# Kernel tuning notes

Hardware: AMD Instinct MI355X
Metric: run time of the kernel (lower is better)

## Reference

```python
import jax, jax.numpy as jnp
import numpy as np

N = 400000      # simplices (edges of the complexes)
E = 2400000     # nnz of each Laplacian
F_IN = 32
H = 64
KAPPA = 3
G = 512         # graphs in batch
N_OUT = 8
EPS = 1e-5


def spmm(edge_index, edge_values, x, n):
    # y[i] = sum_e val_e * x[j],  i = edge_index[0], j = edge_index[1]
    msg = edge_values[:, None] * x[edge_index[1]]
    return jax.ops.segment_sum(msg, edge_index[0], num_segments=n)


def sc_layer(x, li, lv, ui, uv, Wl, bl, Wu, bu, Wh, bh):
    # SCNN layer: z_low + z_up + z_har (aggr_x fused in)
    n = x.shape[0]
    z = x @ Wh + bh                       # harmonic / identity term
    xl = x
    for k in range(KAPPA):
        xl = spmm(li, lv, xl, n)          # L_low^{k+1} x
        z = z + xl @ Wl[k] + bl[k]
    xu = x
    for k in range(KAPPA):
        xu = spmm(ui, uv, xu, n)          # L_up^{k+1} x
        z = z + xu @ Wu[k] + bu[k]
    return z


def batch_norm(x, gamma, beta):
    mean = jnp.mean(x, axis=0)
    var = jnp.mean((x - mean) ** 2, axis=0)   # biased, as torch BN training
    return (x - mean) * jax.lax.rsqrt(var + EPS) * gamma + beta


def setup_inputs() -> dict:
    key = jax.random.key(0)
    ks = jax.random.split(key, 32)
    s_in = 1.0 / np.sqrt(F_IN)
    s_h = 1.0 / np.sqrt(H)
    inp = {
        "x": jax.random.normal(ks[0], (N, F_IN), jnp.float32),
        "lower_edge_index": jax.random.randint(ks[1], (2, E), 0, N),
        "lower_edge_values": jax.random.normal(ks[2], (E,), jnp.float32),
        "upper_edge_index": jax.random.randint(ks[3], (2, E), 0, N),
        "upper_edge_values": jax.random.normal(ks[4], (E,), jnp.float32),
        "batch_index": jnp.sort(jax.random.randint(ks[5], (N,), 0, G)),
        # layer 0 (F_IN -> H)
        "l0_Wl": jax.random.normal(ks[6], (KAPPA, F_IN, H), jnp.float32) * s_in,
        "l0_bl": jnp.zeros((KAPPA, H), jnp.float32),
        "l0_Wu": jax.random.normal(ks[7], (KAPPA, F_IN, H), jnp.float32) * s_in,
        "l0_bu": jnp.zeros((KAPPA, H), jnp.float32),
        "l0_Wh": jax.random.normal(ks[8], (F_IN, H), jnp.float32) * s_in,
        "l0_bh": jnp.zeros((H,), jnp.float32),
        # layer 1 (H -> H)
        "l1_Wl": jax.random.normal(ks[9], (KAPPA, H, H), jnp.float32) * s_h,
        "l1_bl": jnp.zeros((KAPPA, H), jnp.float32),
        "l1_Wu": jax.random.normal(ks[10], (KAPPA, H, H), jnp.float32) * s_h,
        "l1_bu": jnp.zeros((KAPPA, H), jnp.float32),
        "l1_Wh": jax.random.normal(ks[11], (H, H), jnp.float32) * s_h,
        "l1_bh": jnp.zeros((H,), jnp.float32),
        # batch norms
        "bn0_g": jnp.ones((H,), jnp.float32),
        "bn0_b": jnp.zeros((H,), jnp.float32),
        "bn1_g": jnp.ones((H,), jnp.float32),
        "bn1_b": jnp.zeros((H,), jnp.float32),
        # output MLP [2H, H, N_OUT]
        "mlp_W1": jax.random.normal(ks[12], (2 * H, H), jnp.float32) / np.sqrt(2 * H),
        "mlp_b1": jnp.zeros((H,), jnp.float32),
        "mlp_W2": jax.random.normal(ks[13], (H, N_OUT), jnp.float32) * s_h,
        "mlp_b2": jnp.zeros((N_OUT,), jnp.float32),
    }
    return inp


def reference(x, lower_edge_values, upper_edge_values,
              l0_Wl, l0_bl, l0_Wu, l0_bu, l0_Wh, l0_bh,
              l1_Wl, l1_bl, l1_Wu, l1_bu, l1_Wh, l1_bh,
              bn0_g, bn0_b, bn1_g, bn1_b,
              mlp_W1, mlp_b1, mlp_W2, mlp_b2,
              lower_edge_index, upper_edge_index, batch_index):
    li, ui, bi = lower_edge_index, upper_edge_index, batch_index
    lv, uv = lower_edge_values, upper_edge_values

    h = sc_layer(x, li, lv, ui, uv, l0_Wl, l0_bl, l0_Wu, l0_bu, l0_Wh, l0_bh)
    h = jax.nn.elu(batch_norm(h, bn0_g, bn0_b))
    h = sc_layer(h, li, lv, ui, uv, l1_Wl, l1_bl, l1_Wu, l1_bu, l1_Wh, l1_bh)
    h = jax.nn.elu(batch_norm(h, bn1_g, bn1_b))

    # global max pool + global mean pool per graph
    gmax = jax.ops.segment_max(h, bi, num_segments=G)
    gsum = jax.ops.segment_sum(h, bi, num_segments=G)
    cnt = jax.ops.segment_sum(jnp.ones((h.shape[0],), h.dtype), bi, num_segments=G)
    gmean = gsum / jnp.maximum(cnt, 1.0)[:, None]
    g = jax.nn.elu(jnp.concatenate([gmax, gmean], axis=1))  # [G, 2H]

    # MLP [2H -> H -> N_OUT]
    g = jax.nn.relu(g @ mlp_W1 + mlp_b1)
    return g @ mlp_W2 + mlp_b2
```

## Files before the change

kernel.cpp:

```cpp
#include <hip/hip_runtime.h>
#include <hip/hip_bf16.h>
#include <math.h>

#define N_SIMP 400000
#define E_NNZ  2400000
#define FIN    32
#define HDIM   64
#define KAPPA  3
#define G_NUM  512
#define NOUT   8
#define BN_EPS 1e-5

#define NDIG_HALF 391
#define NDIG      782
#define P1_EDGES  16384
#define P1_BLOCKS 293
#define P1_T      1024
#define P1_EPT    16
#define P2_CAP    7168
#define P2_T      512
#define P2_ITERS  14

typedef __hip_bfloat16 bf16;
typedef _Float16 f16;
typedef short s8v __attribute__((ext_vector_type(8)));
typedef ushort u8v __attribute__((ext_vector_type(8)));
typedef _Float16 h8v __attribute__((ext_vector_type(8)));
typedef float f4v __attribute__((ext_vector_type(4)));

__device__ __forceinline__ float elu_f(float x) {
    return x > 0.f ? x : expm1f(x);
}
__device__ __forceinline__ float bf2f(ushort u) {
    return __uint_as_float(((unsigned int)u) << 16);
}
__device__ __forceinline__ ushort f2bf(float f) {
    bf16 h = (bf16)f;
    return *(ushort*)&h;
}


__global__ __launch_bounds__(P1_T, 1) void p1_sort_kernel(
        const int* __restrict__ eiL, const float* __restrict__ lv,
        const int* __restrict__ eiU, const float* __restrict__ uv,
        int* __restrict__ ccnt, int* __restrict__ bofsv,
        int2* __restrict__ coarse) {
    __shared__ int2 rec[P1_EDGES];
    __shared__ int h[NDIG];
    __shared__ int hscan[P1_T];
    int t = threadIdx.x;
    for (int j = t; j < NDIG; j += P1_T) h[j] = 0;
    __syncthreads();
    int base_i = blockIdx.x * P1_EDGES;
    int key[P1_EPT], val[P1_EPT], dg[P1_EPT];
#pragma unroll
    for (int k = 0; k < P1_EPT; ++k) {
        int i = base_i + k * P1_T + t;
        int dd = -1;
        if (i < 2 * E_NNZ) {
            int row, col;
            float v;
            if (i < E_NNZ) {
                row = eiL[i]; col = eiL[E_NNZ + i]; v = lv[i];
                dd = row >> 10;
            } else {
                int e = i - E_NNZ;
                row = eiU[e]; col = eiU[E_NNZ + e]; v = uv[e];
                dd = NDIG_HALF + (row >> 10);
            }
            key[k] = ((row & 1023) << 22) | col;
            val[k] = __float_as_int(v);
            atomicAdd(&h[dd], 1);
        }
        dg[k] = dd;
    }
    __syncthreads();
    int cv = (t < NDIG) ? h[t] : 0;
    hscan[t] = cv;
    __syncthreads();
    for (int off = 1; off < P1_T; off <<= 1) {
        int x = (t >= off) ? hscan[t - off] : 0;
        __syncthreads();
        hscan[t] += x;
        __syncthreads();
    }
    if (t < NDIG) {
        int ex = hscan[t] - cv;
        ccnt[blockIdx.x * NDIG + t] = cv;
        bofsv[blockIdx.x * NDIG + t] = ex;
        h[t] = ex;
    }
    __syncthreads();
#pragma unroll
    for (int k = 0; k < P1_EPT; ++k) {
        if (dg[k] >= 0) {
            int pos = atomicAdd(&h[dg[k]], 1);
            rec[pos] = make_int2(key[k], val[k]);
        }
    }
    __syncthreads();
    int2* dst = coarse + (size_t)blockIdx.x * P1_EDGES;
    int nrec = 2 * E_NNZ - base_i;
    if (nrec > P1_EDGES) nrec = P1_EDGES;
    for (int j = t; j < nrec; j += P1_T) dst[j] = rec[j];
}

__global__ void digit_total_kernel(const int* __restrict__ cnt, int* __restrict__ tot) {
    int d = blockIdx.x * 256 + threadIdx.x;
    if (d >= NDIG) return;
    int run = 0;
    for (int b = 0; b < P1_BLOCKS; ++b) run += cnt[b * NDIG + d];
    tot[d] = run;
}

__global__ __launch_bounds__(1024) void scan_base_kernel(int* __restrict__ tot) {
    __shared__ int s[1024];
    int t = threadIdx.x;
    int v = (t < NDIG) ? tot[t] : 0;
    s[t] = v;
    __syncthreads();
    for (int off = 1; off < 1024; off <<= 1) {
        int x = (t >= off) ? s[t - off] : 0;
        __syncthreads();
        s[t] += x;
        __syncthreads();
    }
    if (t < NDIG) tot[t] = s[t] - v;
    if (t == 1023) tot[NDIG] = s[1023];
}


__global__ __launch_bounds__(P2_T) void p2_build_kernel(
        const int2* __restrict__ coarse, const int* __restrict__ ccnt,
        const int* __restrict__ bofsv, const int* __restrict__ basev,
        int* __restrict__ rpL, int* __restrict__ rpU,
        int2* __restrict__ edgeL, int2* __restrict__ edgeU) {
    __shared__ int pk[P2_CAP];
    __shared__ int vl[P2_CAP];
    __shared__ int hist[1024];
    __shared__ int sc[P2_T];
    __shared__ int fo[P1_BLOCKS];
    __shared__ int stot;
    int d = blockIdx.x;
    int t = threadIdx.x;
    int len = 0, ofs = 0;
    if (t < P1_BLOCKS) { len = ccnt[t * NDIG + d]; ofs = bofsv[t * NDIG + d]; }
    sc[t] = len;
    __syncthreads();
    for (int off = 1; off < P2_T; off <<= 1) {
        int x = (t >= off) ? sc[t - off] : 0;
        __syncthreads();
        sc[t] += x;
        __syncthreads();
    }
    if (t < P1_BLOCKS) { fo[t] = sc[t] - len; hist[t] = len; hist[512 + t] = ofs; }
    if (t == P1_BLOCKS - 1) stot = sc[t];
    __syncthreads();
    int sz = stot;
    if (sz > P2_CAP) sz = P2_CAP;
    int wv = t >> 6, lane = t & 63;
    for (int b = wv; b < P1_BLOCKS; b += P2_T / 64) {
        int L = hist[b], O = hist[512 + b], F = fo[b];
        const int2* sp = coarse + (size_t)b * P1_EDGES + O;
        for (int j = lane; j < L; j += 64) {
            int dst2 = F + j;
            if (dst2 < P2_CAP) {
                int2 r = sp[j];
                pk[dst2] = r.x;
                vl[dst2] = r.y;
            }
        }
    }
    __syncthreads();
    hist[t] = 0;
    hist[t + P2_T] = 0;
    __syncthreads();
    int myrank[P2_ITERS];
#pragma unroll
    for (int k = 0; k < P2_ITERS; ++k) {
        int j = k * P2_T + t;
        myrank[k] = (j < sz) ? atomicAdd(&hist[((unsigned)pk[j]) >> 22], 1) : 0;
    }
    __syncthreads();
    int h0 = hist[2 * t], h1 = hist[2 * t + 1];
    sc[t] = h0 + h1;
    __syncthreads();
    for (int off = 1; off < P2_T; off <<= 1) {
        int x = (t >= off) ? sc[t - off] : 0;
        __syncthreads();
        sc[t] += x;
        __syncthreads();
    }
    int pbase = sc[t] - (h0 + h1);
    __syncthreads();
    hist[2 * t] = pbase;
    hist[2 * t + 1] = pbase + h0;
    int which = (d >= NDIG_HALF);
    int lbase = basev[d] - (which ? E_NNZ : 0);
    int rowbase = (which ? d - NDIG_HALF : d) << 10;
    int* rp = which ? rpU : rpL;
    int r0 = rowbase + 2 * t, r1 = r0 + 1;
    if (r0 < N_SIMP) rp[r0] = lbase + pbase;
    if (r1 < N_SIMP) rp[r1] = lbase + pbase + h0;
    __syncthreads();
    int2* eout = which ? edgeU : edgeL;
#pragma unroll
    for (int k = 0; k < P2_ITERS; ++k) {
        int j = k * P2_T + t;
        if (j < sz) {
            unsigned p = (unsigned)pk[j];
            int pos = lbase + hist[p >> 22] + myrank[k];
            eout[pos] = make_int2((int)(p & 0x3FFFFF), vl[j]);
        }
    }
}


__global__ void combine_bias_kernel(const float* __restrict__ bh,
                                    const float* __restrict__ bl,
                                    const float* __restrict__ bu,
                                    float* __restrict__ out) {
    int h = threadIdx.x;
    float acc = bh[h];
    for (int k = 0; k < KAPPA; ++k) acc += bl[k * HDIM + h] + bu[k * HDIM + h];
    out[h] = acc;
}

__global__ void f32_to_bf16_kernel(const float* __restrict__ in, bf16* __restrict__ out) {
    int idx = blockIdx.x * 256 + threadIdx.x;
    float4 v = ((const float4*)in)[idx];
    ushort4 w;
    w.x = f2bf(v.x); w.y = f2bf(v.y); w.z = f2bf(v.z); w.w = f2bf(v.w);
    ((ushort4*)out)[idx] = w;
}

__global__ void wtrans_all_kernel(const float* __restrict__ s0, const float* __restrict__ s1,
                                  const float* __restrict__ s2, const float* __restrict__ s3,
                                  const float* __restrict__ s4, const float* __restrict__ s5,
                                  ushort* __restrict__ wt) {
    int idx = blockIdx.x * 256 + threadIdx.x;
    const float* src; int off;
    if (idx < 2048)       { src = s0; off = 0; }
    else if (idx < 6144)  { src = s1; off = 2048; }
    else if (idx < 12288) { src = s2; off = 6144; }
    else if (idx < 18432) { src = s3; off = 12288; }
    else if (idx < 30720) { src = s4; off = 18432; }
    else                  { src = s5; off = 30720; }
    int rel = idx - off;
    int frag = rel >> 9;
    int r = rel & 511;
    int lane = r >> 3, j = r & 7;
    int q = lane >> 4, n = lane & 15;
    int ch = frag >> 2, nblk = frag & 3;
    int k = ch * 32 + q * 8 + j;
    int nout = nblk * 16 + n;
    wt[idx] = f2bf(src[k * 64 + nout]);
}


__global__ void spmm32_kernel(const int* __restrict__ rp, const int2* __restrict__ edge,
                              const bf16* __restrict__ srcb, int src_stride,
                              bf16* __restrict__ dstb) {
    const ushort* src = (const ushort*)srcb;
    ushort* dst = (ushort*)dstb;
    int tid = threadIdx.x;
    int lane = tid & 63;
    int wv = tid >> 6;
    int grp = lane >> 2;
    int li = lane & 3;
    int row = blockIdx.x * 64 + wv * 16 + grp;
    int s = rp[row];
    int e = (row == N_SIMP - 1) ? E_NNZ : rp[row + 1];
    int deg = e - s;
    float a[8] = {0.f, 0.f, 0.f, 0.f, 0.f, 0.f, 0.f, 0.f};
    if (deg > 0) {
        int2 ed[8];
#pragma unroll
        for (int t = 0; t < 8; ++t) {
            int j = s + t;
            ed[t] = edge[(j < e) ? j : (e - 1)];
        }
        u8v xs[8];
#pragma unroll
        for (int t = 0; t < 8; ++t)
            xs[t] = *(const u8v*)(src + (size_t)ed[t].x * src_stride + li * 8);
#pragma unroll
        for (int t = 0; t < 8; ++t) {
            float v = (t < deg) ? __int_as_float(ed[t].y) : 0.f;
#pragma unroll
            for (int c = 0; c < 8; ++c) a[c] += v * bf2f(xs[t][c]);
        }
        for (int j = s + 8; j < e; j += 4) {
            int2 e2[4];
#pragma unroll
            for (int t = 0; t < 4; ++t) {
                int jj = j + t;
                e2[t] = edge[(jj < e) ? jj : (e - 1)];
            }
            u8v x2[4];
#pragma unroll
            for (int t = 0; t < 4; ++t)
                x2[t] = *(const u8v*)(src + (size_t)e2[t].x * src_stride + li * 8);
#pragma unroll
            for (int t = 0; t < 4; ++t) {
                float v = (j + t < e) ? __int_as_float(e2[t].y) : 0.f;
#pragma unroll
                for (int c = 0; c < 8; ++c) a[c] += v * bf2f(x2[t][c]);
            }
        }
    }
    u8v w;
#pragma unroll
    for (int c = 0; c < 8; ++c) w[c] = f2bf(a[c]);
    *(u8v*)(dst + (size_t)row * 32 + li * 8) = w;
}

__global__ void spmm64_kernel(const int* __restrict__ rp, const int2* __restrict__ edge,
                              const bf16* __restrict__ srcb, bf16* __restrict__ dstb) {
    const ushort* src = (const ushort*)srcb;
    ushort* dst = (ushort*)dstb;
    int tid = threadIdx.x;
    int lane = tid & 63;
    int wv = tid >> 6;
    int grp = lane >> 3;
    int li = lane & 7;
    int row = blockIdx.x * 32 + wv * 8 + grp;
    int s = rp[row];
    int e = (row == N_SIMP - 1) ? E_NNZ : rp[row + 1];
    int deg = e - s;
    float a[8] = {0.f, 0.f, 0.f, 0.f, 0.f, 0.f, 0.f, 0.f};
    if (deg > 0) {
        int2 ed[8];
#pragma unroll
        for (int t = 0; t < 8; ++t) {
            int j = s + t;
            ed[t] = edge[(j < e) ? j : (e - 1)];
        }
        u8v xs[8];
#pragma unroll
        for (int t = 0; t < 8; ++t)
            xs[t] = *(const u8v*)(src + (size_t)ed[t].x * 64 + li * 8);
#pragma unroll
        for (int t = 0; t < 8; ++t) {
            float v = (t < deg) ? __int_as_float(ed[t].y) : 0.f;
#pragma unroll
            for (int c = 0; c < 8; ++c) a[c] += v * bf2f(xs[t][c]);
        }
        for (int j = s + 8; j < e; j += 4) {
            int2 e2[4];
#pragma unroll
            for (int t = 0; t < 4; ++t) {
                int jj = j + t;
                e2[t] = edge[(jj < e) ? jj : (e - 1)];
            }
            u8v x2[4];
#pragma unroll
            for (int t = 0; t < 4; ++t)
                x2[t] = *(const u8v*)(src + (size_t)e2[t].x * 64 + li * 8);
#pragma unroll
            for (int t = 0; t < 4; ++t) {
                float v = (j + t < e) ? __int_as_float(e2[t].y) : 0.f;
#pragma unroll
                for (int c = 0; c < 8; ++c) a[c] += v * bf2f(x2[t][c]);
            }
        }
    }
    u8v w;
#pragma unroll
    for (int c = 0; c < 8; ++c) w[c] = f2bf(a[c]);
    *(u8v*)(dst + (size_t)row * 64 + li * 8) = w;
}


template <int NCH, int NCH1, bool INIT>
__global__ __launch_bounds__(256) void mfma_gemm_kernel(
        const ushort* __restrict__ s0, int st0,
        const ushort* __restrict__ s1, int st1,
        const ushort* __restrict__ s2, int st2,
        const ushort* __restrict__ s3, int st3,
        const ushort* __restrict__ s4, int st4,
        const ushort* __restrict__ s5, int st5,
        const ushort* __restrict__ Wt1,
        const ushort* __restrict__ Wt2,
        const float* __restrict__ bias,
        f16* __restrict__ z) {
    int tid = threadIdx.x;
    int wv = tid >> 6, lane = tid & 63;
    int quad = lane >> 4, n = lane & 15;
    int rowbase = blockIdx.x * 64 + wv * 16;
    int arow = rowbase + n;

    f4v acc0 = {0.f, 0.f, 0.f, 0.f};
    f4v acc1 = {0.f, 0.f, 0.f, 0.f};
    f4v acc2 = {0.f, 0.f, 0.f, 0.f};
    f4v acc3 = {0.f, 0.f, 0.f, 0.f};

#pragma unroll
    for (int ch = 0; ch < NCH; ++ch) {
        const ushort* sp = (ch == 0) ? s0 : (ch == 1) ? s1 : (ch == 2) ? s2
                         : (ch == 3) ? s3 : (ch == 4) ? s4 : s5;
        int st = (ch == 0) ? st0 : (ch == 1) ? st1 : (ch == 2) ? st2
               : (ch == 3) ? st3 : (ch == 4) ? st4 : st5;
        const ushort* wb = (ch < NCH1) ? (Wt1 + (size_t)ch * 2048)
                                       : (Wt2 + (size_t)(ch - NCH1) * 2048);
        s8v a = *(const s8v*)(sp + (size_t)arow * st + quad * 8);
        const ushort* wq = wb + lane * 8;
        s8v b0 = *(const s8v*)(wq + 0 * 512);
        s8v b1 = *(const s8v*)(wq + 1 * 512);
        s8v b2 = *(const s8v*)(wq + 2 * 512);
        s8v b3 = *(const s8v*)(wq + 3 * 512);
        acc0 = __builtin_amdgcn_mfma_f32_16x16x32_bf16(a, b0, acc0, 0, 0, 0);
        acc1 = __builtin_amdgcn_mfma_f32_16x16x32_bf16(a, b1, acc1, 0, 0, 0);
        acc2 = __builtin_amdgcn_mfma_f32_16x16x32_bf16(a, b2, acc2, 0, 0, 0);
        acc3 = __builtin_amdgcn_mfma_f32_16x16x32_bf16(a, b3, acc3, 0, 0, 0);
    }
#pragma unroll
    for (int r = 0; r < 4; ++r) {
        int orow = rowbase + quad * 4 + r;
        f16* zp = z + (size_t)orow * 64 + n;
        if (INIT) {
            zp[0]  = (f16)(bias[n]      + acc0[r]);
            zp[16] = (f16)(bias[16 + n] + acc1[r]);
            zp[32] = (f16)(bias[32 + n] + acc2[r]);
            zp[48] = (f16)(bias[48 + n] + acc3[r]);
        } else {
            zp[0]  = (f16)((float)zp[0]  + acc0[r]);
            zp[16] = (f16)((float)zp[16] + acc1[r]);
            zp[32] = (f16)((float)zp[32] + acc2[r]);
            zp[48] = (f16)((float)zp[48] + acc3[r]);
        }
    }
}


__global__ void bn_stats_kernel(const f16* __restrict__ z, double* __restrict__ stats) {
    __shared__ float ss[256 * 8], qq[256 * 8];
    int tid = threadIdx.x;
    const h8v* z8 = (const h8v*)z;
    const int total8 = N_SIMP * HDIM / 8;
    float fs[8] = {0, 0, 0, 0, 0, 0, 0, 0};
    float fq[8] = {0, 0, 0, 0, 0, 0, 0, 0};
    for (int i = blockIdx.x * 256 + tid; i < total8; i += (int)gridDim.x * 256) {
        h8v v = z8[i];
#pragma unroll
        for (int c = 0; c < 8; ++c) {
            float f = (float)v[c];
            fs[c] += f;
            fq[c] += f * f;
        }
    }
#pragma unroll
    for (int c = 0; c < 8; ++c) { ss[tid * 8 + c] = fs[c]; qq[tid * 8 + c] = fq[c]; }
    __syncthreads();
    if (tid < 64) {
        int sel = tid >> 3, slot = tid & 7;
        double a = 0.0, b = 0.0;
#pragma unroll 8
        for (int k = 0; k < 32; ++k) {
            int t = sel + (k << 3);
            a += (double)ss[t * 8 + slot];
            b += (double)qq[t * 8 + slot];
        }
        atomicAdd(&stats[tid], a);
        atomicAdd(&stats[64 + tid], b);
    }
}

__global__ void bn_elu_bf16_kernel(const f16* __restrict__ z, const double* __restrict__ stats,
                                   const float* __restrict__ gamma, const float* __restrict__ beta,
                                   bf16* __restrict__ out) {
    __shared__ float scale_s[64], shift_s[64];
    int tid = threadIdx.x;
    if (tid < 64) {
        double mean = stats[tid] / (double)N_SIMP;
        double var = stats[64 + tid] / (double)N_SIMP - mean * mean;
        double sc = (double)gamma[tid] / sqrt(var + BN_EPS);
        scale_s[tid] = (float)sc;
        shift_s[tid] = (float)((double)beta[tid] - mean * sc);
    }
    __syncthreads();
    const h8v* z8 = (const h8v*)z;
    u8v* o8 = (u8v*)out;
    const int total8 = N_SIMP * HDIM / 8;
    int hb = (tid & 7) * 8;
    for (int i = blockIdx.x * 256 + tid; i < total8; i += (int)gridDim.x * 256) {
        h8v v = z8[i];
        u8v w;
#pragma unroll
        for (int c = 0; c < 8; ++c)
            w[c] = f2bf(elu_f((float)v[c] * scale_s[hb + c] + shift_s[hb + c]));
        o8[i] = w;
    }
}

__global__ void pool_bn_kernel(const f16* __restrict__ zbuf, const int* __restrict__ bidx,
                               const double* __restrict__ stats,
                               const float* __restrict__ gamma, const float* __restrict__ beta,
                               float* __restrict__ gbuf) {
    __shared__ float scale_s[64], shift_s[64];
    __shared__ float pmax[256 * 8], psum[256 * 8];
    int tid = threadIdx.x;
    if (tid < 64) {
        double mean = stats[tid] / (double)N_SIMP;
        double var = stats[64 + tid] / (double)N_SIMP - mean * mean;
        double sc = (double)gamma[tid] / sqrt(var + BN_EPS);
        scale_s[tid] = (float)sc;
        shift_s[tid] = (float)((double)beta[tid] - mean * sc);
    }
    __syncthreads();
    int g = blockIdx.x;
    int lo = 0, hi = N_SIMP;
    while (lo < hi) { int mid = (lo + hi) >> 1; if (bidx[mid] < g) lo = mid + 1; else hi = mid; }
    int start = lo;
    hi = N_SIMP;
    while (lo < hi) { int mid = (lo + hi) >> 1; if (bidx[mid] < g + 1) lo = mid + 1; else hi = mid; }
    int end = lo;
    int li = tid & 7;
    int rr = tid >> 3;
    const h8v* z8 = (const h8v*)zbuf;
    float mx[8], sm[8];
#pragma unroll
    for (int c = 0; c < 8; ++c) { mx[c] = -INFINITY; sm[c] = 0.f; }
    float sc8[8], sh8[8];
#pragma unroll
    for (int c = 0; c < 8; ++c) { sc8[c] = scale_s[li * 8 + c]; sh8[c] = shift_s[li * 8 + c]; }
    for (int i = start + rr; i < end; i += 32) {
        h8v v = z8[(size_t)i * 8 + li];
#pragma unroll
        for (int c = 0; c < 8; ++c) {
            float y = elu_f((float)v[c] * sc8[c] + sh8[c]);
            mx[c] = fmaxf(mx[c], y);
            sm[c] += y;
        }
    }
#pragma unroll
    for (int c = 0; c < 8; ++c) { pmax[tid * 8 + c] = mx[c]; psum[tid * 8 + c] = sm[c]; }
    __syncthreads();
    if (tid < 64) {
        int sel = tid >> 3, slot = tid & 7;
        float m = -INFINITY, s = 0.f;
#pragma unroll 8
        for (int k = 0; k < 32; ++k) {
            int t = k * 8 + sel;
            m = fmaxf(m, pmax[t * 8 + slot]);
            s += psum[t * 8 + slot];
        }
        int cnt = end - start;
        float mean = s / fmaxf((float)cnt, 1.f);
        gbuf[g * 128 + tid] = elu_f(m);
        gbuf[g * 128 + 64 + tid] = elu_f(mean);
    }
}

__global__ void mlp_kernel(const float* __restrict__ gbuf, const float* __restrict__ W1,
                           const float* __restrict__ b1, const float* __restrict__ W2,
                           const float* __restrict__ b2, float* __restrict__ out) {
    __shared__ float gs[128];
    __shared__ float hs[64];
    int g = blockIdx.x, tid = threadIdx.x;
    gs[tid] = gbuf[g * 128 + tid];
    gs[64 + tid] = gbuf[g * 128 + 64 + tid];
    __syncthreads();
    float acc = b1[tid];
#pragma unroll
    for (int k = 0; k < 128; ++k) acc += gs[k] * W1[k * 64 + tid];
    hs[tid] = fmaxf(acc, 0.f);
    __syncthreads();
    if (tid < 8) {
        float o = b2[tid];
#pragma unroll
        for (int k = 0; k < 64; ++k) o += hs[k] * W2[k * 8 + tid];
        out[g * 8 + tid] = o;
    }
}


extern "C" void kernel_launch(void* const* d_in, const int* in_sizes, int n_in,
                              void* d_out, int out_size, void* d_ws, size_t ws_size,
                              hipStream_t stream) {
    const float* x     = (const float*)d_in[0];
    const int*   li    = (const int*)d_in[1];
    const float* lv    = (const float*)d_in[2];
    const int*   ui    = (const int*)d_in[3];
    const float* uv    = (const float*)d_in[4];
    const int*   bidx  = (const int*)d_in[5];
    const float* l0_Wl = (const float*)d_in[6];
    const float* l0_bl = (const float*)d_in[7];
    const float* l0_Wu = (const float*)d_in[8];
    const float* l0_bu = (const float*)d_in[9];
    const float* l0_Wh = (const float*)d_in[10];
    const float* l0_bh = (const float*)d_in[11];
    const float* l1_Wl = (const float*)d_in[12];
    const float* l1_bl = (const float*)d_in[13];
    const float* l1_Wu = (const float*)d_in[14];
    const float* l1_bu = (const float*)d_in[15];
    const float* l1_Wh = (const float*)d_in[16];
    const float* l1_bh = (const float*)d_in[17];
    const float* bn0_g = (const float*)d_in[18];
    const float* bn0_b = (const float*)d_in[19];
    const float* bn1_g = (const float*)d_in[20];
    const float* bn1_b = (const float*)d_in[21];
    const float* mW1   = (const float*)d_in[22];
    const float* mb1   = (const float*)d_in[23];
    const float* mW2   = (const float*)d_in[24];
    const float* mb2   = (const float*)d_in[25];
    float* out = (float*)d_out;

    char* base = (char*)d_ws;
    f16*   z     = (f16*)base;
    bf16*  h0bf  = (bf16*)(base + 51200000ull);
    bf16*  g1    = (bf16*)(base + 102400000ull);
    bf16*  g2    = (bf16*)(base + 153600000ull);
    int2*  edgeL = (int2*)(base + 204800000ull);
    int2*  edgeU = (int2*)(base + 224000000ull);
    int*   rpL   = (int*)(base + 243200000ull);
    int*   rpU   = (int*)(base + 244800032ull);
    double* stats = (double*)(base + 246404160ull);
    float* cbias  = (float*)(base + 246405184ull);
    float* gbuf   = (float*)(base + 246405440ull);
    ushort* wt    = (ushort*)(base + 246667584ull);

    int2* coarse = (int2*)base;
    int*  basev  = (int*)(base + 38500000ull);
    int*  ccnt   = (int*)(base + 51200000ull);
    int*  bofsv  = (int*)(base + 52200000ull);

    bf16* xbf  = g1;
    bf16* cAL  = g1 + (size_t)N_SIMP * 32;
    bf16* cBL  = g2;
    bf16* cCL  = g2 + (size_t)N_SIMP * 32;
    bf16* cAU  = h0bf;
    bf16* cBU  = h0bf + (size_t)N_SIMP * 32;
    bf16* cCU  = g1;

    ushort* wt_l0h = wt;
    ushort* wt_l1h = wt + 2048;
    ushort* wt_l0l = wt + 6144;
    ushort* wt_l0u = wt + 12288;
    ushort* wt_l1l = wt + 18432;
    ushort* wt_l1u = wt + 30720;

    const int SP32_BLOCKS = N_SIMP / 64;
    const int SP64_BLOCKS = N_SIMP / 32;
    const int MF_BLOCKS   = N_SIMP / 64;

    wtrans_all_kernel<<<168, 256, 0, stream>>>(l0_Wh, l1_Wh, l0_Wl, l0_Wu, l1_Wl, l1_Wu, wt);
    f32_to_bf16_kernel<<<N_SIMP * 32 / 4 / 256, 256, 0, stream>>>(x, xbf);

    p1_sort_kernel<<<P1_BLOCKS, P1_T, 0, stream>>>(li, lv, ui, uv, ccnt, bofsv, coarse);
    digit_total_kernel<<<(NDIG + 255) / 256, 256, 0, stream>>>(ccnt, basev);
    scan_base_kernel<<<1, 1024, 0, stream>>>(basev);
    p2_build_kernel<<<NDIG, P2_T, 0, stream>>>(coarse, ccnt, bofsv, basev,
                                               rpL, rpU, edgeL, edgeU);

    const ushort* xbfu = (const ushort*)xbf;
    const ushort* h0u  = (const ushort*)h0bf;
    const ushort* g1u  = (const ushort*)g1;
    const ushort* g2u  = (const ushort*)g2;

    combine_bias_kernel<<<1, 64, 0, stream>>>(l0_bh, l0_bl, l0_bu, cbias);
    mfma_gemm_kernel<1, 1, true><<<MF_BLOCKS, 256, 0, stream>>>(
        xbfu, 32, nullptr, 0, nullptr, 0, nullptr, 0, nullptr, 0, nullptr, 0,
        wt_l0h, wt_l0h, cbias, z);

    spmm32_kernel<<<SP32_BLOCKS, 256, 0, stream>>>(rpL, edgeL, xbf, 32, cAL);
    spmm32_kernel<<<SP32_BLOCKS, 256, 0, stream>>>(rpL, edgeL, cAL, 32, cBL);
    spmm32_kernel<<<SP32_BLOCKS, 256, 0, stream>>>(rpL, edgeL, cBL, 32, cCL);
    spmm32_kernel<<<SP32_BLOCKS, 256, 0, stream>>>(rpU, edgeU, xbf, 32, cAU);
    spmm32_kernel<<<SP32_BLOCKS, 256, 0, stream>>>(rpU, edgeU, cAU, 32, cBU);
    spmm32_kernel<<<SP32_BLOCKS, 256, 0, stream>>>(rpU, edgeU, cBU, 32, cCU);
    mfma_gemm_kernel<6, 3, false><<<MF_BLOCKS, 256, 0, stream>>>(
        (const ushort*)cAL, 32, (const ushort*)cBL, 32, (const ushort*)cCL, 32,
        (const ushort*)cAU, 32, (const ushort*)cBU, 32, (const ushort*)cCU, 32,
        wt_l0l, wt_l0u, nullptr, z);

    (void)hipMemsetAsync(stats, 0, 128 * sizeof(double), stream);
    bn_stats_kernel<<<1024, 256, 0, stream>>>(z, stats);
    bn_elu_bf16_kernel<<<1024, 256, 0, stream>>>(z, stats, bn0_g, bn0_b, h0bf);

    combine_bias_kernel<<<1, 64, 0, stream>>>(l1_bh, l1_bl, l1_bu, cbias);

    spmm64_kernel<<<SP64_BLOCKS, 256, 0, stream>>>(rpL, edgeL, h0bf, g1);
    spmm64_kernel<<<SP64_BLOCKS, 256, 0, stream>>>(rpL, edgeL, g1, g2);
    mfma_gemm_kernel<6, 2, true><<<MF_BLOCKS, 256, 0, stream>>>(
        h0u, 64, h0u + 32, 64, g1u, 64, g1u + 32, 64, g2u, 64, g2u + 32, 64,
        wt_l1h, wt_l1l, cbias, z);
    spmm64_kernel<<<SP64_BLOCKS, 256, 0, stream>>>(rpL, edgeL, g2, g1);
    spmm64_kernel<<<SP64_BLOCKS, 256, 0, stream>>>(rpU, edgeU, h0bf, g2);
    mfma_gemm_kernel<4, 2, false><<<MF_BLOCKS, 256, 0, stream>>>(
        g1u, 64, g1u + 32, 64, g2u, 64, g2u + 32, 64, nullptr, 0, nullptr, 0,
        wt_l1l + 4 * 2048, wt_l1u, nullptr, z);
    spmm64_kernel<<<SP64_BLOCKS, 256, 0, stream>>>(rpU, edgeU, g2, g1);
    spmm64_kernel<<<SP64_BLOCKS, 256, 0, stream>>>(rpU, edgeU, g1, g2);
    mfma_gemm_kernel<4, 4, false><<<MF_BLOCKS, 256, 0, stream>>>(
        g1u, 64, g1u + 32, 64, g2u, 64, g2u + 32, 64, nullptr, 0, nullptr, 0,
        wt_l1u + 2 * 2048, wt_l1u + 2 * 2048, nullptr, z);

    (void)hipMemsetAsync(stats, 0, 128 * sizeof(double), stream);
    bn_stats_kernel<<<1024, 256, 0, stream>>>(z, stats);

    pool_bn_kernel<<<G_NUM, 256, 0, stream>>>(z, bidx, stats, bn1_g, bn1_b, gbuf);
    mlp_kernel<<<G_NUM, 64, 0, stream>>>(gbuf, mW1, mb1, mW2, mb2, out);
}
```

Measured before the change: 1.197 ms.

## Fuse BN statistics into final GEMM epilogues and halve sort block size

Batch-norm sum and sum-of-squares are now accumulated in the epilogue of the last MFMA GEMM of each layer, using shared-memory float atomics and then global double atomics. This drops both bn_stats_kernel launches and their full re-read of z. Separately, the coarse sort pass uses 8192-edge blocks (586 blocks) without the single-block occupancy bound, and the build kernel gathers each bucket with 8-lane groups. The fused stats add atomic contention in every GEMM block, and the smaller sort blocks double the per-digit bucket metadata.

New measurement: 1.368 ms. +14.3%, slower.

```diff
diff --git a/kernel.cpp b/kernel.cpp
--- a/kernel.cpp
+++ b/kernel.cpp
@@ -13,10 +13,10 @@
 
 #define NDIG_HALF 391
 #define NDIG      782
-#define P1_EDGES  16384
-#define P1_BLOCKS 293
+#define P1_EDGES  8192
+#define P1_BLOCKS 586
 #define P1_T      1024
-#define P1_EPT    16
+#define P1_EPT    8
 #define P2_CAP    7168
 #define P2_T      512
 #define P2_ITERS  14
@@ -40,7 +40,7 @@
 }
 
 
-__global__ __launch_bounds__(P1_T, 1) void p1_sort_kernel(
+__global__ __launch_bounds__(P1_T) void p1_sort_kernel(
         const int* __restrict__ eiL, const float* __restrict__ lv,
         const int* __restrict__ eiU, const float* __restrict__ uv,
         int* __restrict__ ccnt, int* __restrict__ bofsv,
@@ -139,13 +139,17 @@
     __shared__ int vl[P2_CAP];
     __shared__ int hist[1024];
     __shared__ int sc[P2_T];
+    __shared__ int flen[P1_BLOCKS];
+    __shared__ int fofs[P1_BLOCKS];
     __shared__ int fo[P1_BLOCKS];
     __shared__ int stot;
     int d = blockIdx.x;
     int t = threadIdx.x;
-    int len = 0, ofs = 0;
-    if (t < P1_BLOCKS) { len = ccnt[t * NDIG + d]; ofs = bofsv[t * NDIG + d]; }
-    sc[t] = len;
+    int f0 = 2 * t, f1 = 2 * t + 1;
+    int L0 = 0, L1 = 0, O0 = 0, O1 = 0;
+    if (f0 < P1_BLOCKS) { L0 = ccnt[f0 * NDIG + d]; O0 = bofsv[f0 * NDIG + d]; }
+    if (f1 < P1_BLOCKS) { L1 = ccnt[f1 * NDIG + d]; O1 = bofsv[f1 * NDIG + d]; }
+    sc[t] = L0 + L1;
     __syncthreads();
     for (int off = 1; off < P2_T; off <<= 1) {
         int x = (t >= off) ? sc[t - off] : 0;
@@ -153,16 +157,19 @@
         sc[t] += x;
         __syncthreads();
     }
-    if (t < P1_BLOCKS) { fo[t] = sc[t] - len; hist[t] = len; hist[512 + t] = ofs; }
-    if (t == P1_BLOCKS - 1) stot = sc[t];
+    int pb = sc[t] - (L0 + L1);
+    if (f0 < P1_BLOCKS) { flen[f0] = L0; fofs[f0] = O0; fo[f0] = pb; }
+    if (f1 < P1_BLOCKS) { flen[f1] = L1; fofs[f1] = O1; fo[f1] = pb + L0; }
+    if (t == P2_T - 1) stot = sc[t];
     __syncthreads();
     int sz = stot;
     if (sz > P2_CAP) sz = P2_CAP;
     int wv = t >> 6, lane = t & 63;
-    for (int b = wv; b < P1_BLOCKS; b += P2_T / 64) {
-        int L = hist[b], O = hist[512 + b], F = fo[b];
+    int grp8 = lane >> 3, l8 = lane & 7;
+    for (int b = wv * 8 + grp8; b < P1_BLOCKS; b += 64) {
+        int L = flen[b], O = fofs[b], F = fo[b];
         const int2* sp = coarse + (size_t)b * P1_EDGES + O;
-        for (int j = lane; j < L; j += 64) {
+        for (int j = l8; j < L; j += 8) {
             int dst2 = F + j;
             if (dst2 < P2_CAP) {
                 int2 r = sp[j];
@@ -372,7 +379,7 @@
 }
 
 
-template <int NCH, int NCH1, bool INIT>
+template <int NCH, int NCH1, bool INIT, bool STATS>
 __global__ __launch_bounds__(256) void mfma_gemm_kernel(
         const ushort* __restrict__ s0, int st0,
         const ushort* __restrict__ s1, int st1,
@@ -383,12 +390,19 @@
         const ushort* __restrict__ Wt1,
         const ushort* __restrict__ Wt2,
         const float* __restrict__ bias,
+        double* __restrict__ stats,
         f16* __restrict__ z) {
+    __shared__ float s_sum[64], s_sq[64];
     int tid = threadIdx.x;
     int wv = tid >> 6, lane = tid & 63;
     int quad = lane >> 4, n = lane & 15;
     int rowbase = blockIdx.x * 64 + wv * 16;
     int arow = rowbase + n;
+
+    if (STATS) {
+        if (tid < 64) { s_sum[tid] = 0.f; s_sq[tid] = 0.f; }
+        __syncthreads();
+    }
 
     f4v acc0 = {0.f, 0.f, 0.f, 0.f};
     f4v acc1 = {0.f, 0.f, 0.f, 0.f};
@@ -414,57 +428,47 @@
         acc2 = __builtin_amdgcn_mfma_f32_16x16x32_bf16(a, b2, acc2, 0, 0, 0);
         acc3 = __builtin_amdgcn_mfma_f32_16x16x32_bf16(a, b3, acc3, 0, 0, 0);
     }
+    float fs[4] = {0.f, 0.f, 0.f, 0.f};
+    float fq[4] = {0.f, 0.f, 0.f, 0.f};
 #pragma unroll
     for (int r = 0; r < 4; ++r) {
         int orow = rowbase + quad * 4 + r;
         f16* zp = z + (size_t)orow * 64 + n;
+        f16 w0, w1, w2, w3;
         if (INIT) {
-            zp[0]  = (f16)(bias[n]      + acc0[r]);
-            zp[16] = (f16)(bias[16 + n] + acc1[r]);
-            zp[32] = (f16)(bias[32 + n] + acc2[r]);
-            zp[48] = (f16)(bias[48 + n] + acc3[r]);
+            w0 = (f16)(bias[n]      + acc0[r]);
+            w1 = (f16)(bias[16 + n] + acc1[r]);
+            w2 = (f16)(bias[32 + n] + acc2[r]);
+            w3 = (f16)(bias[48 + n] + acc3[r]);
         } else {
-            zp[0]  = (f16)((float)zp[0]  + acc0[r]);
-            zp[16] = (f16)((float)zp[16] + acc1[r]);
-            zp[32] = (f16)((float)zp[32] + acc2[r]);
-            zp[48] = (f16)((float)zp[48] + acc3[r]);
-        }
-    }
-}
-
-
-__global__ void bn_stats_kernel(const f16* __restrict__ z, double* __restrict__ stats) {
-    __shared__ float ss[256 * 8], qq[256 * 8];
-    int tid = threadIdx.x;
-    const h8v* z8 = (const h8v*)z;
-    const int total8 = N_SIMP * HDIM / 8;
-    float fs[8] = {0, 0, 0, 0, 0, 0, 0, 0};
-    float fq[8] = {0, 0, 0, 0, 0, 0, 0, 0};
-    for (int i = blockIdx.x * 256 + tid; i < total8; i += (int)gridDim.x * 256) {
-        h8v v = z8[i];
-#pragma unroll
-        for (int c = 0; c < 8; ++c) {
-            float f = (float)v[c];
-            fs[c] += f;
-            fq[c] += f * f;
-        }
-    }
-#pragma unroll
-    for (int c = 0; c < 8; ++c) { ss[tid * 8 + c] = fs[c]; qq[tid * 8 + c] = fq[c]; }
-    __syncthreads();
-    if (tid < 64) {
-        int sel = tid >> 3, slot = tid & 7;
-        double a = 0.0, b = 0.0;
-#pragma unroll 8
-        for (int k = 0; k < 32; ++k) {
-            int t = sel + (k << 3);
-            a += (double)ss[t * 8 + slot];
-            b += (double)qq[t * 8 + slot];
-        }
-        atomicAdd(&stats[tid], a);
-        atomicAdd(&stats[64 + tid], b);
-    }
-}
+            w0 = (f16)((float)zp[0]  + acc0[r]);
+            w1 = (f16)((float)zp[16] + acc1[r]);
+            w2 = (f16)((float)zp[32] + acc2[r]);
+            w3 = (f16)((float)zp[48] + acc3[r]);
+        }
+        zp[0] = w0; zp[16] = w1; zp[32] = w2; zp[48] = w3;
+        if (STATS) {
+            float v0 = (float)w0, v1 = (float)w1, v2 = (float)w2, v3 = (float)w3;
+            fs[0] += v0; fq[0] += v0 * v0;
+            fs[1] += v1; fq[1] += v1 * v1;
+            fs[2] += v2; fq[2] += v2 * v2;
+            fs[3] += v3; fq[3] += v3 * v3;
+        }
+    }
+    if (STATS) {
+#pragma unroll
+        for (int k = 0; k < 4; ++k) {
+            atomicAdd(&s_sum[k * 16 + n], fs[k]);
+            atomicAdd(&s_sq[k * 16 + n], fq[k]);
+        }
+        __syncthreads();
+        if (tid < 64) {
+            atomicAdd(&stats[tid], (double)s_sum[tid]);
+            atomicAdd(&stats[64 + tid], (double)s_sq[tid]);
+        }
+    }
+}
+
 
 __global__ void bn_elu_bf16_kernel(const f16* __restrict__ z, const double* __restrict__ stats,
                                    const float* __restrict__ gamma, const float* __restrict__ beta,
@@ -623,7 +627,7 @@
     int2* coarse = (int2*)base;
     int*  basev  = (int*)(base + 38500000ull);
     int*  ccnt   = (int*)(base + 51200000ull);
-    int*  bofsv  = (int*)(base + 52200000ull);
+    int*  bofsv  = (int*)(base + 53100000ull);
 
     bf16* xbf  = g1;
     bf16* cAL  = g1 + (size_t)N_SIMP * 32;
@@ -659,9 +663,10 @@
     const ushort* g2u  = (const ushort*)g2;
 
     combine_bias_kernel<<<1, 64, 0, stream>>>(l0_bh, l0_bl, l0_bu, cbias);
-    mfma_gemm_kernel<1, 1, true><<<MF_BLOCKS, 256, 0, stream>>>(
+    (void)hipMemsetAsync(stats, 0, 128 * sizeof(double), stream);
+    mfma_gemm_kernel<1, 1, true, false><<<MF_BLOCKS, 256, 0, stream>>>(
         xbfu, 32, nullptr, 0, nullptr, 0, nullptr, 0, nullptr, 0, nullptr, 0,
-        wt_l0h, wt_l0h, cbias, z);
+        wt_l0h, wt_l0h, cbias, nullptr, z);
 
     spmm32_kernel<<<SP32_BLOCKS, 256, 0, stream>>>(rpL, edgeL, xbf, 32, cAL);
     spmm32_kernel<<<SP32_BLOCKS, 256, 0, stream>>>(rpL, edgeL, cAL, 32, cBL);
@@ -669,35 +674,31 @@
     spmm32_kernel<<<SP32_BLOCKS, 256, 0, stream>>>(rpU, edgeU, xbf, 32, cAU);
     spmm32_kernel<<<SP32_BLOCKS, 256, 0, stream>>>(rpU, edgeU, cAU, 32, cBU);
     spmm32_kernel<<<SP32_BLOCKS, 256, 0, stream>>>(rpU, edgeU, cBU, 32, cCU);
-    mfma_gemm_kernel<6, 3, false><<<MF_BLOCKS, 256, 0, stream>>>(
+    mfma_gemm_kernel<6, 3, false, true><<<MF_BLOCKS, 256, 0, stream>>>(
         (const ushort*)cAL, 32, (const ushort*)cBL, 32, (const ushort*)cCL, 32,
         (const ushort*)cAU, 32, (const ushort*)cBU, 32, (const ushort*)cCU, 32,
-        wt_l0l, wt_l0u, nullptr, z);
-
+        wt_l0l, wt_l0u, nullptr, stats, z);
+
+    bn_elu_bf16_kernel<<<1024, 256, 0, stream>>>(z, stats, bn0_g, bn0_b, h0bf);
+
+    combine_bias_kernel<<<1, 64, 0, stream>>>(l1_bh, l1_bl, l1_bu, cbias);
     (void)hipMemsetAsync(stats, 0, 128 * sizeof(double), stream);
-    bn_stats_kernel<<<1024, 256, 0, stream>>>(z, stats);
-    bn_elu_bf16_kernel<<<1024, 256, 0, stream>>>(z, stats, bn0_g, bn0_b, h0bf);
-
-    combine_bias_kernel<<<1, 64, 0, stream>>>(l1_bh, l1_bl, l1_bu, cbias);
 
     spmm64_kernel<<<SP64_BLOCKS, 256, 0, stream>>>(rpL, edgeL, h0bf, g1);
     spmm64_kernel<<<SP64_BLOCKS, 256, 0, stream>>>(rpL, edgeL, g1, g2);
-    mfma_gemm_kernel<6, 2, true><<<MF_BLOCKS, 256, 0, stream>>>(
+    mfma_gemm_kernel<6, 2, true, false><<<MF_BLOCKS, 256, 0, stream>>>(
         h0u, 64, h0u + 32, 64, g1u, 64, g1u + 32, 64, g2u, 64, g2u + 32, 64,
-        wt_l1h, wt_l1l, cbias, z);
+        wt_l1h, wt_l1l, cbias, nullptr, z);
     spmm64_kernel<<<SP64_BLOCKS, 256, 0, stream>>>(rpL, edgeL, g2, g1);
     spmm64_kernel<<<SP64_BLOCKS, 256, 0, stream>>>(rpU, edgeU, h0bf, g2);
-    mfma_gemm_kernel<4, 2, false><<<MF_BLOCKS, 256, 0, stream>>>(
+    mfma_gemm_kernel<4, 2, false, false><<<MF_BLOCKS, 256, 0, stream>>>(
         g1u, 64, g1u + 32, 64, g2u, 64, g2u + 32, 64, nullptr, 0, nullptr, 0,
-        wt_l1l + 4 * 2048, wt_l1u, nullptr, z);
+        wt_l1l + 4 * 2048, wt_l1u, nullptr, nullptr, z);
     spmm64_kernel<<<SP64_BLOCKS, 256, 0, stream>>>(rpU, edgeU, g2, g1);
     spmm64_kernel<<<SP64_BLOCKS, 256, 0, stream>>>(rpU, edgeU, g1, g2);
-    mfma_gemm_kernel<4, 4, false><<<MF_BLOCKS, 256, 0, stream>>>(
+    mfma_gemm_kernel<4, 4, false, true><<<MF_BLOCKS, 256, 0, stream>>>(
         g1u, 64, g1u + 32, 64, g2u, 64, g2u + 32, 64, nullptr, 0, nullptr, 0,
-        wt_l1u + 2 * 2048, wt_l1u + 2 * 2048, nullptr, z);
-
-    (void)hipMemsetAsync(stats, 0, 128 * sizeof(double), stream);
-    bn_stats_kernel<<<1024, 256, 0, stream>>>(z, stats);
+        wt_l1u + 2 * 2048, wt_l1u + 2 * 2048, nullptr, stats, z);
 
     pool_bn_kernel<<<G_NUM, 256, 0, stream>>>(z, bidx, stats, bn1_g, bn1_b, gbuf);
     mlp_kernel<<<G_NUM, 64, 0, stream>>>(gbuf, mW1, mb1, mW2, mb2, out);
```
